# Kernel tuning notes

Measured on AMD Instinct MI355X. Metric: run time of the kernel, lower is better.

The kernel has to match this reference:

```python
import jax, jax.numpy as jnp
import numpy as np

# Module hyperparameters (from init_kwargs)
KH = KW = 3
STRIDE = 2
PAD = 1
OUT_PAD = 1
DIL = 1
IN_LEN = 8   # length of each input capsule
OUT_LEN = 8  # length of each output capsule
N_IN_CAPS = 64 // IN_LEN    # 8
N_OUT_CAPS = 64 // OUT_LEN  # 8
NUM_ITERATIONS = 3


def _squash(x):
    # v * |v|^2 / ((1 + |v|^2) * |v|), along last (capsule-length) dim
    sn = jnp.sum(x * x, axis=-1, keepdims=True)
    return x * (sn / ((1.0 + sn) * jnp.sqrt(sn + 1e-12)))


def _k_means_routing(priors, num_iterations):
    # priors: [..., K, M] ; soft k-means routing with 'dot' similarity,
    # softmax over the votes dim K (softmax_dim=-2), squash at the end.
    out = jnp.mean(priors, axis=-2, keepdims=True)          # [..., 1, M]
    for _ in range(num_iterations):
        nrm = jnp.linalg.norm(out, axis=-1, keepdims=True)
        out_n = out / jnp.maximum(nrm, 1e-12)               # F.normalize(p=2)
        logits = jnp.sum(priors * out_n, axis=-1, keepdims=True)  # [..., K, 1]
        probs = jax.nn.softmax(logits, axis=-2)
        out = jnp.sum(probs * priors, axis=-2, keepdims=True)
    return _squash(out)[..., 0, :]                          # [..., M]


def setup_inputs() -> dict:
    key = jax.random.key(0)
    k1, k2, k3 = jax.random.split(key, 3)
    input = jax.random.normal(k1, (2, 64, 32, 32), dtype=jnp.float32)
    # weight: (in_length, out_channels//out_length, out_length, kh, kw)
    weight = jax.random.normal(k2, (IN_LEN, N_OUT_CAPS, OUT_LEN, KH, KW), dtype=jnp.float32) * 0.1
    # bias: (out_channels//out_length, out_length)
    bias = jax.random.normal(k3, (N_OUT_CAPS, OUT_LEN), dtype=jnp.float32) * 0.1
    return {"input": input, "weight": weight, "bias": bias}


def reference(input, weight, bias):
    n, c_in, h_in, w_in = input.shape
    fi = c_in // IN_LEN
    fo = weight.shape[1]
    # conv_transpose == conv(lhs-dilated input, spatially flipped kernel)
    pad_lo = DIL * (KH - 1) - PAD
    patches = jax.lax.conv_general_dilated_patches(
        input, (KH, KW), (1, 1),
        padding=((pad_lo, pad_lo + OUT_PAD), (pad_lo, pad_lo + OUT_PAD)),
        lhs_dilation=(STRIDE, STRIDE), rhs_dilation=(DIL, DIL))
    ho, wo = patches.shape[-2], patches.shape[-1]
    # feature dim of patches is ordered (c, kh, kw), channel-major
    patches = patches.reshape(n, fi, IN_LEN, KH, KW, ho, wo)
    w_flip = weight[..., ::-1, ::-1]  # [IN_LEN, fo, OUT_LEN, KH, KW]
    # votes: each (input capsule, kernel tap) casts a vote per output capsule
    priors = jnp.einsum('nflhwpq,lgmhw->npqgfhwm', patches, w_flip)
    priors = priors.reshape(n, ho, wo, fo, fi * KH * KW, OUT_LEN)
    out = _k_means_routing(priors, NUM_ITERATIONS)  # [n, ho, wo, fo, OUT_LEN]
    out = out + bias                                # bias: [fo, OUT_LEN]
    out = out.reshape(n, ho, wo, fo * OUT_LEN).transpose(0, 3, 1, 2)
    return out  # [n, out_channels, ho, wo] = [2, 64, 64, 64]
```

## Files before the change

### kernel.cpp

```cpp
#include <hip/hip_runtime.h>
#include <math.h>

#define HIN 32
#define WIN 32
#define NITER 3
#define TIN_ELEMS 131072

__global__ __launch_bounds__(256) void prep(const float* __restrict__ in,
                                            const float* __restrict__ weight,
                                            float* __restrict__ tin,
                                            float* __restrict__ wprep) {
    __shared__ float lds[64 * 33];
    const int b = blockIdx.x;
    const int t = threadIdx.x;
    if (b < 64) {
        const int n = b >> 5;
        const int s0 = (b & 31) << 5;
        const float* ib = in + n * 65536;
        float* ob = tin + n * 65536;
#pragma unroll
        for (int k = 0; k < 8; ++k) {
            int idx = k * 256 + t;
            int c = idx >> 5, sl = idx & 31;
            lds[c * 33 + sl] = ib[c * 1024 + s0 + sl];
        }
        __syncthreads();
#pragma unroll
        for (int k = 0; k < 8; ++k) {
            int idx = k * 256 + t;
            int sl = idx >> 6, c = idx & 63;
            ob[(size_t)(s0 + sl) * 64 + c] = lds[c * 33 + sl];
        }
    } else {
#pragma unroll
        for (int k = 0; k < 2; ++k) {
            const int lgm = k * 256 + t;
            const int l = lgm >> 6, g = (lgm >> 3) & 7, m = lgm & 7;
            const float* src = weight + lgm * 9;
            float* drow = wprep + g * 64 + ((m + g) & 7) * 8 + l;
#pragma unroll
            for (int kh = 0; kh < 3; ++kh)
#pragma unroll
                for (int kw = 0; kw < 3; ++kw) {
                    const int tap = (2 - kh) * 3 + (2 - kw);
                    drow[tap * 512] = src[kh * 3 + kw];
                }
        }
    }
}

template <int CTRL>
__device__ __forceinline__ float dpp_add(float v) {
    int p = __builtin_amdgcn_update_dpp(0, __float_as_int(v), CTRL, 0xF, 0xF, true);
    return v + __int_as_float(p);
}
__device__ __forceinline__ float sum8(float v) {
    v = dpp_add<0xB1>(v);
    v = dpp_add<0x4E>(v);
    v = dpp_add<0x141>(v);
    return v;
}

template <int TH, int TW>
__device__ __forceinline__ void run_path(
    const float* __restrict__ tin, const float* __restrict__ wprep,
    const float* __restrict__ bias, float* __restrict__ out,
    float* __restrict__ wlds, float* __restrict__ olds,
    int t, int n, int p, int qb) {
    constexpr int T = TH * TW;
    constexpr float Z = (float)(72 - 8 * T);

    const int wave = t >> 6;
    const int lane = t & 63;

    if (wave < T) {
        const int hh = (TH == 1) ? 1 : ((TW == 2 ? (wave >> 1) : wave) * 2);
        const int ww = (TW == 1) ? 1 : ((wave & 1) * 2);
        const float4* src = (const float4*)(wprep + (hh * 3 + ww) * 512 + lane * 8);
        float4 a = src[0], b2 = src[1];
        float4* dst = (float4*)(wlds + wave * 512 + lane * 8);
        dst[0] = a;
        dst[1] = b2;
    }
    __syncthreads();

    const int g = lane >> 3;
    const int s = lane & 7;
    const int q = qb + 2 * wave;

    float pri[T][8];
#pragma unroll
    for (int i = 0; i < TH; ++i) {
        const int h = (TH == 1) ? 1 : i * 2;
        const int y = (p + h - 1) >> 1;
#pragma unroll
        for (int j = 0; j < TW; ++j) {
            const int v = i * TW + j;
            const int w = (TW == 1) ? 1 : j * 2;
            const int x = (q + w - 1) >> 1;
            const bool valid = (y < HIN) && (x < WIN);
            if (valid) {
                float xv[8];
                const float4* xp =
                    (const float4*)(tin + (((size_t)n * HIN + y) * WIN + x) * 64 + s * 8);
                float4 x0 = xp[0], x1 = xp[1];
                xv[0] = x0.x; xv[1] = x0.y; xv[2] = x0.z; xv[3] = x0.w;
                xv[4] = x1.x; xv[5] = x1.y; xv[6] = x1.z; xv[7] = x1.w;
                const float* wb = wlds + (v * 8 + g) * 64;
#pragma unroll
                for (int m = 0; m < 8; ++m) {
                    const float4* wp = (const float4*)(wb + ((m + g) & 7) * 8);
                    float4 w0 = wp[0], w1 = wp[1];
                    pri[v][m] = xv[0] * w0.x + xv[1] * w0.y + xv[2] * w0.z + xv[3] * w0.w +
                                xv[4] * w1.x + xv[5] * w1.y + xv[6] * w1.z + xv[7] * w1.w;
                }
            } else {
#pragma unroll
                for (int m = 0; m < 8; ++m) pri[v][m] = 0.f;
            }
        }
    }

    float r[9];
#pragma unroll
    for (int m = 0; m < 8; ++m) {
        float a = 0.f;
#pragma unroll
        for (int v = 0; v < T; ++v) a += pri[v][m];
        r[m] = sum8(a);
    }
    r[8] = (float)T * 8.f;

#pragma unroll
    for (int it = 0; it < NITER; ++it) {
        float sn = 0.f;
#pragma unroll
        for (int m = 0; m < 8; ++m) sn += r[m] * r[m];
        const float inv = __builtin_amdgcn_rsqf(fmaxf(sn, 1e-24f));
        float on[8];
#pragma unroll
        for (int m = 0; m < 8; ++m) on[m] = r[m] * inv;

        float acc[9];
        acc[8] = 0.f;
        float e[T];
#pragma unroll
        for (int v = 0; v < T; ++v) {
            float a = 0.f;
#pragma unroll
            for (int m = 0; m < 8; ++m) a += pri[v][m] * on[m];
            e[v] = __expf(a);
            acc[8] += e[v];
        }
#pragma unroll
        for (int m = 0; m < 8; ++m) {
            float a = 0.f;
#pragma unroll
            for (int v = 0; v < T; ++v) a += e[v] * pri[v][m];
            acc[m] = a;
        }
#pragma unroll
        for (int j = 0; j < 9; ++j) r[j] = sum8(acc[j]);
    }

    const float invs = __builtin_amdgcn_rcpf(r[8] + Z);
    float o[8];
#pragma unroll
    for (int m = 0; m < 8; ++m) o[m] = r[m] * invs;

    float sn = 0.f;
#pragma unroll
    for (int m = 0; m < 8; ++m) sn += o[m] * o[m];
    const float factor =
        sn * __builtin_amdgcn_rcpf(1.f + sn) * __builtin_amdgcn_rsqf(sn + 1e-12f);

    float val = o[0];
#pragma unroll
    for (int m = 1; m < 8; ++m)
        if (s == m) val = o[m];
    val = val * factor + bias[g * 8 + s];

    olds[lane * 5 + wave] = val;

    __syncthreads();
    const int c2 = t >> 2, w = t & 3;
    out[(((size_t)n * 64 + c2) * 64 + p) * 64 + qb + 2 * w] = olds[c2 * 5 + w];
}

__global__ __launch_bounds__(256) void caps_routing(
    const float* __restrict__ tin, const float* __restrict__ wprep,
    const float* __restrict__ bias, float* __restrict__ out) {
    __shared__ float wlds[4 * 512];
    __shared__ float olds[64 * 5];
    const int t = threadIdx.x;

    const int b = blockIdx.x;
    const int n = b >> 10;
    const int p = (b >> 4) & 63;
    const int j = b & 15;
    const int qpar = j >> 3;
    const int qb = (j & 7) * 8 + qpar;

    if (p & 1) {
        if (qpar)
            run_path<2, 2>(tin, wprep, bias, out, wlds, olds, t, n, p, qb);
        else
            run_path<2, 1>(tin, wprep, bias, out, wlds, olds, t, n, p, qb);
    } else {
        if (qpar)
            run_path<1, 2>(tin, wprep, bias, out, wlds, olds, t, n, p, qb);
        else
            run_path<1, 1>(tin, wprep, bias, out, wlds, olds, t, n, p, qb);
    }
}

extern "C" void kernel_launch(void* const* d_in, const int* in_sizes, int n_in,
                              void* d_out, int out_size, void* d_ws, size_t ws_size,
                              hipStream_t stream) {
    const float* in = (const float*)d_in[0];
    const float* weight = (const float*)d_in[1];
    const float* bias = (const float*)d_in[2];
    float* out = (float*)d_out;
    float* tin = (float*)d_ws;
    float* wprep = (float*)d_ws + TIN_ELEMS;

    prep<<<65, 256, 0, stream>>>(in, weight, tin, wprep);
    caps_routing<<<2048, 256, 0, stream>>>(tin, wprep, bias, out);
}
```

Before: 74.56 us.

## Vectorize capsule vote and routing math with packed float2 FMAs and padded weight layout

Rewrites the per-lane vote computation and k-means routing iterations to use two-wide float vectors with elementwise FMA, so the compiler can emit packed FP32 instructions (v_pk_fma_f32). The prepared weight layout is changed to interleave output-capsule pairs with padded rows (stride 20/80/640) to match paired m access and reduce LDS bank conflicts. The softmax denominator reduction is now done only on the last iteration. The cost is a larger LDS weight tile and a more complex weight staging loop.

```diff
diff --git a/kernel.cpp b/kernel.cpp
--- a/kernel.cpp
+++ b/kernel.cpp
@@ -5,6 +5,10 @@
 #define WIN 32
 #define NITER 3
 #define TIN_ELEMS 131072
+
+typedef float f2 __attribute__((ext_vector_type(2)));
+__device__ __forceinline__ f2 mk2(float a, float b) { f2 r; r.x = a; r.y = b; return r; }
+__device__ __forceinline__ f2 fma2(f2 a, f2 b, f2 c) { return __builtin_elementwise_fma(a, b, c); }
 
 __global__ __launch_bounds__(256) void prep(const float* __restrict__ in,
                                             const float* __restrict__ weight,
@@ -36,14 +40,15 @@
         for (int k = 0; k < 2; ++k) {
             const int lgm = k * 256 + t;
             const int l = lgm >> 6, g = (lgm >> 3) & 7, m = lgm & 7;
+            const int m2 = m >> 1, h = m & 1;
             const float* src = weight + lgm * 9;
-            float* drow = wprep + g * 64 + ((m + g) & 7) * 8 + l;
+            float* base = wprep + g * 80 + ((m2 + g) & 3) * 20 + l * 2 + h;
 #pragma unroll
             for (int kh = 0; kh < 3; ++kh)
 #pragma unroll
                 for (int kw = 0; kw < 3; ++kw) {
                     const int tap = (2 - kh) * 3 + (2 - kw);
-                    drow[tap * 512] = src[kh * 3 + kw];
+                    base[tap * 640] = src[kh * 3 + kw];
                 }
         }
     }
@@ -76,11 +81,13 @@
     if (wave < T) {
         const int hh = (TH == 1) ? 1 : ((TW == 2 ? (wave >> 1) : wave) * 2);
         const int ww = (TW == 1) ? 1 : ((wave & 1) * 2);
-        const float4* src = (const float4*)(wprep + (hh * 3 + ww) * 512 + lane * 8);
-        float4 a = src[0], b2 = src[1];
-        float4* dst = (float4*)(wlds + wave * 512 + lane * 8);
-        dst[0] = a;
-        dst[1] = b2;
+        const float4* src = (const float4*)(wprep + (hh * 3 + ww) * 640);
+        float4* dst = (float4*)(wlds + wave * 640);
+#pragma unroll
+        for (int k = 0; k < 3; ++k) {
+            const int idx = k * 64 + lane;
+            if (k < 2 || lane < 32) dst[idx] = src[idx];
+        }
     }
     __syncthreads();
 
@@ -88,7 +95,7 @@
     const int s = lane & 7;
     const int q = qb + 2 * wave;
 
-    float pri[T][8];
+    f2 pri2[T][4];
 #pragma unroll
     for (int i = 0; i < TH; ++i) {
         const int h = (TH == 1) ? 1 : i * 2;
@@ -100,84 +107,94 @@
             const int x = (q + w - 1) >> 1;
             const bool valid = (y < HIN) && (x < WIN);
             if (valid) {
-                float xv[8];
                 const float4* xp =
                     (const float4*)(tin + (((size_t)n * HIN + y) * WIN + x) * 64 + s * 8);
                 float4 x0 = xp[0], x1 = xp[1];
-                xv[0] = x0.x; xv[1] = x0.y; xv[2] = x0.z; xv[3] = x0.w;
-                xv[4] = x1.x; xv[5] = x1.y; xv[6] = x1.z; xv[7] = x1.w;
-                const float* wb = wlds + (v * 8 + g) * 64;
-#pragma unroll
-                for (int m = 0; m < 8; ++m) {
-                    const float4* wp = (const float4*)(wb + ((m + g) & 7) * 8);
-                    float4 w0 = wp[0], w1 = wp[1];
-                    pri[v][m] = xv[0] * w0.x + xv[1] * w0.y + xv[2] * w0.z + xv[3] * w0.w +
-                                xv[4] * w1.x + xv[5] * w1.y + xv[6] * w1.z + xv[7] * w1.w;
+                float xv[8] = {x0.x, x0.y, x0.z, x0.w, x1.x, x1.y, x1.z, x1.w};
+                const float* wb = wlds + v * 640 + g * 80;
+#pragma unroll
+                for (int m2 = 0; m2 < 4; ++m2) {
+                    const float4* row = (const float4*)(wb + ((m2 + g) & 3) * 20);
+                    f2 acc = mk2(0.f, 0.f);
+#pragma unroll
+                    for (int k = 0; k < 4; ++k) {
+                        float4 w4 = row[k];
+                        acc = fma2(mk2(xv[2 * k], xv[2 * k]), mk2(w4.x, w4.y), acc);
+                        acc = fma2(mk2(xv[2 * k + 1], xv[2 * k + 1]), mk2(w4.z, w4.w), acc);
+                    }
+                    pri2[v][m2] = acc;
                 }
             } else {
 #pragma unroll
-                for (int m = 0; m < 8; ++m) pri[v][m] = 0.f;
+                for (int m2 = 0; m2 < 4; ++m2) pri2[v][m2] = mk2(0.f, 0.f);
             }
         }
     }
 
-    float r[9];
-#pragma unroll
-    for (int m = 0; m < 8; ++m) {
-        float a = 0.f;
-#pragma unroll
-        for (int v = 0; v < T; ++v) a += pri[v][m];
-        r[m] = sum8(a);
-    }
-    r[8] = (float)T * 8.f;
-
+    f2 rr[4];
+#pragma unroll
+    for (int m2 = 0; m2 < 4; ++m2) {
+        f2 a = mk2(0.f, 0.f);
+#pragma unroll
+        for (int v = 0; v < T; ++v) a += pri2[v][m2];
+        rr[m2].x = sum8(a.x);
+        rr[m2].y = sum8(a.y);
+    }
+
+    float r8v = 0.f;
 #pragma unroll
     for (int it = 0; it < NITER; ++it) {
-        float sn = 0.f;
-#pragma unroll
-        for (int m = 0; m < 8; ++m) sn += r[m] * r[m];
+        f2 t2 = mk2(0.f, 0.f);
+#pragma unroll
+        for (int m2 = 0; m2 < 4; ++m2) t2 = fma2(rr[m2], rr[m2], t2);
+        const float sn = t2.x + t2.y;
         const float inv = __builtin_amdgcn_rsqf(fmaxf(sn, 1e-24f));
-        float on[8];
-#pragma unroll
-        for (int m = 0; m < 8; ++m) on[m] = r[m] * inv;
-
-        float acc[9];
-        acc[8] = 0.f;
-        float e[T];
+        const f2 inv2 = mk2(inv, inv);
+        f2 on2[4];
+#pragma unroll
+        for (int m2 = 0; m2 < 4; ++m2) on2[m2] = rr[m2] * inv2;
+
+        float a8 = 0.f;
+        f2 acc2[4];
+#pragma unroll
+        for (int m2 = 0; m2 < 4; ++m2) acc2[m2] = mk2(0.f, 0.f);
 #pragma unroll
         for (int v = 0; v < T; ++v) {
-            float a = 0.f;
-#pragma unroll
-            for (int m = 0; m < 8; ++m) a += pri[v][m] * on[m];
-            e[v] = __expf(a);
-            acc[8] += e[v];
-        }
-#pragma unroll
-        for (int m = 0; m < 8; ++m) {
-            float a = 0.f;
-#pragma unroll
-            for (int v = 0; v < T; ++v) a += e[v] * pri[v][m];
-            acc[m] = a;
-        }
-#pragma unroll
-        for (int j = 0; j < 9; ++j) r[j] = sum8(acc[j]);
-    }
-
-    const float invs = __builtin_amdgcn_rcpf(r[8] + Z);
-    float o[8];
-#pragma unroll
-    for (int m = 0; m < 8; ++m) o[m] = r[m] * invs;
-
-    float sn = 0.f;
-#pragma unroll
-    for (int m = 0; m < 8; ++m) sn += o[m] * o[m];
+            f2 d2 = mk2(0.f, 0.f);
+#pragma unroll
+            for (int m2 = 0; m2 < 4; ++m2) d2 = fma2(pri2[v][m2], on2[m2], d2);
+            const float e = __expf(d2.x + d2.y);
+            a8 += e;
+            const f2 e2 = mk2(e, e);
+#pragma unroll
+            for (int m2 = 0; m2 < 4; ++m2) acc2[m2] = fma2(e2, pri2[v][m2], acc2[m2]);
+        }
+#pragma unroll
+        for (int m2 = 0; m2 < 4; ++m2) {
+            rr[m2].x = sum8(acc2[m2].x);
+            rr[m2].y = sum8(acc2[m2].y);
+        }
+        if (it == NITER - 1) r8v = sum8(a8);
+    }
+
+    const float invs = __builtin_amdgcn_rcpf(r8v + Z);
+    const f2 invs2 = mk2(invs, invs);
+    f2 o2[4];
+#pragma unroll
+    for (int m2 = 0; m2 < 4; ++m2) o2[m2] = rr[m2] * invs2;
+
+    f2 s2 = mk2(0.f, 0.f);
+#pragma unroll
+    for (int m2 = 0; m2 < 4; ++m2) s2 = fma2(o2[m2], o2[m2], s2);
+    const float sn = s2.x + s2.y;
     const float factor =
         sn * __builtin_amdgcn_rcpf(1.f + sn) * __builtin_amdgcn_rsqf(sn + 1e-12f);
 
-    float val = o[0];
-#pragma unroll
-    for (int m = 1; m < 8; ++m)
-        if (s == m) val = o[m];
+    f2 osel = o2[0];
+#pragma unroll
+    for (int m2 = 1; m2 < 4; ++m2)
+        if ((s >> 1) == m2) osel = o2[m2];
+    float val = (s & 1) ? osel.y : osel.x;
     val = val * factor + bias[g * 8 + s];
 
     olds[lane * 5 + wave] = val;
@@ -190,7 +207,7 @@
 __global__ __launch_bounds__(256) void caps_routing(
     const float* __restrict__ tin, const float* __restrict__ wprep,
     const float* __restrict__ bias, float* __restrict__ out) {
-    __shared__ float wlds[4 * 512];
+    __shared__ float wlds[4 * 640];
     __shared__ float olds[64 * 5];
     const int t = threadIdx.x;
 
```

Result: faster. 69.74 us (-6.5%).
